# Optimization experiments

Measured on AMD Instinct MI355X. Metric: run time of the kernel, lower is better.

## Reference

```python
import jax, jax.numpy as jnp
import numpy as np

B, S, D, H = 4, 2048, 1024, 16
HD = D // H
EPS = 1e-7  # K.epsilon()


def setup_inputs() -> dict:
    key = jax.random.key(0)
    ks = jax.random.split(key, 5)
    scale = 1.0 / np.sqrt(D)  # keep projections numerically tame (glorot-ish)
    return {
        "x": jax.random.normal(ks[0], (B, S, D), dtype=jnp.float32),
        "Wq": jax.random.normal(ks[1], (D, D), dtype=jnp.float32) * scale,
        "bq": jnp.zeros((D,), dtype=jnp.float32),
        "Wk": jax.random.normal(ks[2], (D, D), dtype=jnp.float32) * scale,
        "bk": jnp.zeros((D,), dtype=jnp.float32),
        "Wv": jax.random.normal(ks[3], (D, D), dtype=jnp.float32) * scale,
        "bv": jnp.zeros((D,), dtype=jnp.float32),
        "Wo": jax.random.normal(ks[4], (D, D), dtype=jnp.float32) * scale,
        "bo": jnp.zeros((D,), dtype=jnp.float32),
    }


def _split_heads(t):
    # [B,S,D] -> [B,H,S,HD]
    return t.reshape(B, S, H, HD).transpose(0, 2, 1, 3)


def reference(x, Wq, bq, Wk, bk, Wv, bv, Wo, bo):
    relu = jax.nn.relu
    # projections with post-activation (keras layer applies activation to each mapping)
    q = _split_heads(relu(x @ Wq + bq))
    k = _split_heads(relu(x @ Wk + bk))
    v = _split_heads(relu(x @ Wv + bv))
    # scaled dot-product scores, scale = sqrt(head_dim)
    e = jnp.einsum("bhqd,bhkd->bhqk", q, k) / jnp.sqrt(jnp.asarray(HD, x.dtype))
    # exp with row max over ALL keys (before masking), as in the source
    e = jnp.exp(e - jnp.max(e, axis=-1, keepdims=True))
    # history_only: multiplicative causal mask applied AFTER exp
    causal = (jnp.arange(S)[None, :] <= jnp.arange(S)[:, None]).astype(x.dtype)
    e = e * causal  # broadcasts over [B,H,S,S]
    a = e / (jnp.sum(e, axis=-1, keepdims=True) + EPS)
    ctx = jnp.einsum("bhqk,bhkd->bhqd", a, v)
    y = ctx.transpose(0, 2, 1, 3).reshape(B, S, D)  # merge heads
    return relu(y @ Wo + bo)
```

## Files before the change

kernel.cpp:

```cpp
#include <hip/hip_runtime.h>
#include <hip/hip_bf16.h>
#include <cstdint>
#include <cstddef>

#define B_  4
#define S_  2048
#define D_  1024
#define H_  16
#define HD_ 64

typedef _Float16 half8  __attribute__((ext_vector_type(8)));
typedef _Float16 half4v __attribute__((ext_vector_type(4)));
typedef _Float16 half2v __attribute__((ext_vector_type(2)));
typedef float    f32x4  __attribute__((ext_vector_type(4)));
typedef unsigned int uint2v __attribute__((ext_vector_type(2)));
typedef unsigned int uint4v __attribute__((ext_vector_type(4)));

__device__ __forceinline__ void async_copy16(const void* g, void* l) {
    __builtin_amdgcn_global_load_lds(
        (const __attribute__((address_space(1))) unsigned int*)g,
        (__attribute__((address_space(3))) unsigned int*)l,
        16, 0, 0);
}

__device__ __forceinline__ half8 hscale8(half8 v, _Float16 s) {
    #pragma unroll
    for (int i = 0; i < 8; ++i) v[i] *= s;
    return v;
}

__device__ __forceinline__ unsigned int pack2(float a, float b) {
    half2v h = { (_Float16)a, (_Float16)b };
    return __builtin_bit_cast(unsigned int, h);
}


__global__ void cast_x_kernel(const float4* __restrict__ in, half4v* __restrict__ out, int n4) {
    int i = blockIdx.x * 256 + threadIdx.x;
    if (i < n4) {
        float4 v = in[i];
        half4v h = { (_Float16)v.x, (_Float16)v.y, (_Float16)v.z, (_Float16)v.w };
        out[i] = h;
    }
}

__global__ void transpose_cast4_kernel(
    const float* __restrict__ W0, const float* __restrict__ W1,
    const float* __restrict__ W2, const float* __restrict__ W3,
    _Float16* __restrict__ T0, _Float16* __restrict__ T1,
    _Float16* __restrict__ T2, _Float16* __restrict__ T3)
{
    __shared__ float tile[32][33];
    const float* Wsel[4] = { W0, W1, W2, W3 };
    _Float16*    Tsel[4] = { T0, T1, T2, T3 };
    const float* W  = Wsel[blockIdx.z];
    _Float16*    Wt = Tsel[blockIdx.z];
    const int bn = blockIdx.x * 32, bk = blockIdx.y * 32;
    const int tx = threadIdx.x, ty = threadIdx.y;
    #pragma unroll
    for (int i = 0; i < 32; i += 8)
        tile[ty + i][tx] = W[(size_t)(bk + ty + i) * D_ + bn + tx];
    __syncthreads();
    #pragma unroll
    for (int i = 0; i < 32; i += 8)
        Wt[(size_t)(bn + ty + i) * D_ + bk + tx] = (_Float16)tile[tx][ty + i];
}

template<int OUT_MODE>
__global__ __launch_bounds__(256, 2) void gemm_bt_kernel(
    const _Float16* __restrict__ A, const _Float16* __restrict__ Bt,
    const float* __restrict__ b0, const float* __restrict__ b1,
    const float* __restrict__ b2,
    void* __restrict__ C0, void* __restrict__ C1, void* __restrict__ C2,
    int M, int N, int K)
{
    __shared__ _Float16 As[128 * 64];
    __shared__ _Float16 Bs[128 * 64];
    const int tid  = threadIdx.x;
    const int wid  = tid >> 6, lane = tid & 63;
    const int lr   = lane & 15, lq = lane >> 4;
    const int m0   = blockIdx.x * 128, n0 = blockIdx.y * 128;
    const int wm   = (wid >> 1) * 64, wn = (wid & 1) * 64;
    const int srow = tid >> 3;
    const int csw  = ((tid & 7) ^ (srow & 7)) * 8;

    f32x4 acc[4][4] = {};

    for (int k0 = 0; k0 < K; k0 += 64) {
        __syncthreads();
        #pragma unroll
        for (int i = 0; i < 4; ++i) {
            async_copy16(A  + (size_t)(m0 + i * 32 + srow) * K + k0 + csw,
                         (char*)As + (i * 256 + wid * 64) * 16);
            async_copy16(Bt + (size_t)(n0 + i * 32 + srow) * K + k0 + csw,
                         (char*)Bs + (i * 256 + wid * 64) * 16);
        }
        __syncthreads();
        #pragma unroll
        for (int ks = 0; ks < 2; ++ks) {
            half8 af[4], bf[4];
            #pragma unroll
            for (int t = 0; t < 4; ++t) {
                af[t] = *(const half8*)(As + (wm + t * 16 + lr) * 64 + (((ks * 4 + lq) ^ (lr & 7)) * 8));
                bf[t] = *(const half8*)(Bs + (wn + t * 16 + lr) * 64 + (((ks * 4 + lq) ^ (lr & 7)) * 8));
            }
            #pragma unroll
            for (int mt = 0; mt < 4; ++mt)
                #pragma unroll
                for (int nt = 0; nt < 4; ++nt)
                    acc[mt][nt] = __builtin_amdgcn_mfma_f32_16x16x32_f16(
                        af[mt], bf[nt], acc[mt][nt], 0, 0, 0);
        }
    }

    const int seg = (OUT_MODE == 3) ? (n0 >> 10) : 0;
    const float* bp = (OUT_MODE == 3) ? (seg == 0 ? b0 : (seg == 1 ? b1 : b2)) : b0;

    #pragma unroll
    for (int mt = 0; mt < 4; ++mt) {
        const int row = m0 + wm + mt * 16 + lq * 4;
        #pragma unroll
        for (int nt = 0; nt < 4; ++nt) {
            const int col = n0 + wn + nt * 16 + lr;
            const int cl  = (OUT_MODE == 3) ? (col & 1023) : col;
            const float bb = bp[cl];
            if (OUT_MODE == 3 && seg == 2) {
                const int b = row >> 11, sq = row & 2047;
                const int h = cl >> 6, hd = cl & 63;
                half4v o;
                #pragma unroll
                for (int r = 0; r < 4; ++r) {
                    float v = acc[mt][nt][r] + bb;
                    o[r] = (_Float16)(v > 0.0f ? v : 0.0f);
                }
                *(half4v*)((_Float16*)C2 +
                           ((size_t)(b * 16 + h) * 64 + hd) * S_ + sq) = o;
            } else if (OUT_MODE == 3) {
                _Float16* dst = (_Float16*)(seg ? C1 : C0);
                #pragma unroll
                for (int r = 0; r < 4; ++r) {
                    float v = acc[mt][nt][r] + bb;
                    dst[(size_t)(row + r) * 1024 + cl] = (_Float16)(v > 0.0f ? v : 0.0f);
                }
            } else {
                #pragma unroll
                for (int r = 0; r < 4; ++r) {
                    float v = acc[mt][nt][r] + bb;
                    ((float*)C0)[(size_t)(row + r) * N + col] = v > 0.0f ? v : 0.0f;
                }
            }
        }
    }
}

__global__ __launch_bounds__(256, 3) void attn_kernel(
    const _Float16* __restrict__ Qg, const _Float16* __restrict__ Kg,
    const _Float16* __restrict__ Vtg, _Float16* __restrict__ Y)
{
    __shared__ _Float16 Ks[2][64 * 64];
    __shared__ _Float16 Vt[2][64 * 64];

    const int i  = blockIdx.x;
    const int bh = ((i & 7) << 3) | (i >> 7);
    const int tp = (i >> 3) & 15;
    const int b  = bh >> 4, h = bh & 15;
    const int tid = threadIdx.x, wid = tid >> 6, lane = tid & 63;
    const int lr = lane & 15, lq = lane >> 4;

    const size_t base  = ((size_t)b * S_) * D_ + (size_t)h * HD_;
    const _Float16* Vh = Vtg + (size_t)bh * 64 * S_;

    const int srow = tid >> 3;
    const int csw  = ((tid & 7) ^ (srow & 7)) * 8;

    const int qb[2] = { 64 * tp + 16 * wid, 2048 - 64 * (tp + 1) + 16 * wid };
    const int dk[2] = { tp, 31 - tp };
    const int nIter = 32 - tp;

    half8 aq[2][2];
    #pragma unroll
    for (int f = 0; f < 2; ++f) {
        const _Float16* qp = Qg + base + (size_t)(qb[f] + lr) * D_;
        aq[f][0] = hscale8(*(const half8*)(qp + lq * 8),      (_Float16)0.18033688f);
        aq[f][1] = hscale8(*(const half8*)(qp + 32 + lq * 8), (_Float16)0.18033688f);
    }

    float lsum[2] = {};
    f32x4 O[2][4] = {};
    half8 apf[2][2];

    auto issue_tile = [&](int kb) {
        const int bufi = kb & 1;
        #pragma unroll
        for (int ii = 0; ii < 2; ++ii) {
            async_copy16(Kg + base + (size_t)(kb * 64 + ii * 32 + srow) * D_ + csw,
                         (char*)Ks[bufi] + (ii * 256 + wid * 64) * 16);
            async_copy16(Vh + (size_t)(ii * 32 + srow) * S_ + kb * 64 + csw,
                         (char*)Vt[bufi] + (ii * 256 + wid * 64) * 16);
        }
    };

    issue_tile(0);

    for (int kb = 0; kb < nIter; ++kb) {
        const int cur = kb & 1;
        __syncthreads();
        if (kb + 1 < nIter) issue_tile(kb + 1);

        const _Float16* Kc = Ks[cur];
        const _Float16* Vc = Vt[cur];

        half8 kf[2][4];
        #pragma unroll
        for (int ks = 0; ks < 2; ++ks)
            #pragma unroll
            for (int tt = 0; tt < 4; ++tt)
                kf[ks][tt] = *(const half8*)(Kc + (tt * 16 + lr) * 64 + (((ks * 4 + lq) ^ (lr & 7)) * 8));

        #pragma unroll
        for (int f = 0; f < 2; ++f) {
            if (kb > dk[f]) continue;

            f32x4 sc[4] = {};
            #pragma unroll
            for (int ks = 0; ks < 2; ++ks)
                #pragma unroll
                for (int tt = 0; tt < 4; ++tt)
                    sc[tt] = __builtin_amdgcn_mfma_f32_16x16x32_f16(kf[ks][tt], aq[f][ks], sc[tt], 0, 0, 0);

            const bool diag = (kb == dk[f]);
            const int qg = qb[f] + lr;
            const int kbase = kb * 64 + lq * 4;
            float sum = 0.0f;
            unsigned int pk[4][2];
            #pragma unroll
            for (int tt = 0; tt < 4; ++tt) {
                float ev[4];
                #pragma unroll
                for (int r = 0; r < 4; ++r) {
                    float e = __builtin_amdgcn_exp2f(fminf(sc[tt][r] - 5.770780f, 15.8696f));
                    if (diag)
                        e = (kbase + tt * 16 + r <= qg) ? e : 0.0f;
                    ev[r] = e;
                    sum += e;
                }
                pk[tt][0] = pack2(ev[0], ev[1]);
                pk[tt][1] = pack2(ev[2], ev[3]);
            }
            lsum[f] += sum;

            #pragma unroll
            for (int ks = 0; ks < 2; ++ks) {
                uint2v s1 = __builtin_amdgcn_permlane32_swap(pk[2 * ks][0], pk[2 * ks + 1][0], false, false);
                uint2v s2 = __builtin_amdgcn_permlane16_swap(s1[0], s1[1], false, false);
                uint2v u1 = __builtin_amdgcn_permlane32_swap(pk[2 * ks][1], pk[2 * ks + 1][1], false, false);
                uint2v u2 = __builtin_amdgcn_permlane16_swap(u1[0], u1[1], false, false);
                uint4v d = { s2[0], u2[0], s2[1], u2[1] };
                apf[f][ks] = __builtin_bit_cast(half8, d);
            }
        }

        half8 bv[2][4];
        #pragma unroll
        for (int ks = 0; ks < 2; ++ks)
            #pragma unroll
            for (int tt = 0; tt < 4; ++tt)
                bv[ks][tt] = *(const half8*)(Vc + (tt * 16 + lr) * 64 + (((ks * 4 + lq) ^ (lr & 7)) * 8));

        #pragma unroll
        for (int f = 0; f < 2; ++f) {
            if (kb > dk[f]) continue;
            #pragma unroll
            for (int ks = 0; ks < 2; ++ks)
                #pragma unroll
                for (int tt = 0; tt < 4; ++tt)
                    O[f][tt] = __builtin_amdgcn_mfma_f32_16x16x32_f16(apf[f][ks], bv[ks][tt], O[f][tt], 0, 0, 0);
        }
    }

    #pragma unroll
    for (int f = 0; f < 2; ++f) {
        float tot = lsum[f];
        tot += __shfl_xor(tot, 16);
        tot += __shfl_xor(tot, 32);
        const int q0 = qb[f] + lq * 4;
        #pragma unroll
        for (int r = 0; r < 4; ++r) {
            const float inv = 1.0f / (__shfl(tot, lq * 4 + r) + 1e-7f);
            #pragma unroll
            for (int nt = 0; nt < 4; ++nt)
                Y[base + (size_t)(q0 + r) * D_ + nt * 16 + lr] = (_Float16)(O[f][nt][r] * inv);
        }
    }
}


extern "C" void kernel_launch(void* const* d_in, const int* in_sizes, int n_in,
                              void* d_out, int out_size, void* d_ws, size_t ws_size,
                              hipStream_t stream) {
    const float* x  = (const float*)d_in[0];
    const float* Wq = (const float*)d_in[1];
    const float* bq = (const float*)d_in[2];
    const float* Wk = (const float*)d_in[3];
    const float* bk = (const float*)d_in[4];
    const float* Wv = (const float*)d_in[5];
    const float* bv = (const float*)d_in[6];
    const float* Wo = (const float*)d_in[7];
    const float* bo = (const float*)d_in[8];

    char* ws = (char*)d_ws;
    _Float16* xh  = (_Float16*)ws;
    _Float16* wtq = (_Float16*)(ws + (size_t)16777216);
    _Float16* wtk = wtq + 1048576;
    _Float16* wtv = wtk + 1048576;
    _Float16* wto = wtv + 1048576;
    _Float16* Qh  = (_Float16*)(ws + (size_t)16777216 + 4 * (size_t)2097152);
    _Float16* Kh  = Qh + 8388608;
    _Float16* Vth = Kh + 8388608;
    _Float16* Yh  = Vth + 8388608;
    float* out = (float*)d_out;

    cast_x_kernel<<<8192, 256, 0, stream>>>((const float4*)x, (half4v*)xh, 2097152);
    transpose_cast4_kernel<<<dim3(32, 32, 4), dim3(32, 8), 0, stream>>>(
        Wq, Wk, Wv, Wo, wtq, wtk, wtv, wto);

    gemm_bt_kernel<3><<<dim3(64, 24), 256, 0, stream>>>(
        xh, wtq, bq, bk, bv, Qh, Kh, Vth, 8192, 3072, 1024);

    attn_kernel<<<1024, 256, 0, stream>>>(Qh, Kh, Vth, Yh);

    gemm_bt_kernel<0><<<dim3(64, 8), 256, 0, stream>>>(
        Yh, wto, bo, bo, bo, out, out, out, 8192, 1024, 1024);
}
```

Baseline: 252.9 us.

## Process four query tiles per attention block to reuse K/V tiles

Each attention block now handles four 16-row query fragments per wave (two low and two high causal-paired tiles) instead of two, halving the grid to 512 blocks and sharing every loaded K/V LDS tile across twice the query work. The V fragment loads are hoisted alongside K, the PV MFMA is fused into the per-fragment loop, and s_setprio brackets the MFMA bursts. This cuts global/LDS traffic per unit of work but raises register pressure (launch bounds relaxed from 3 to 2 waves per SIMD) and gives fewer blocks for load balancing.

```diff
diff --git a/kernel.cpp b/kernel.cpp
--- a/kernel.cpp
+++ b/kernel.cpp
@@ -153,7 +153,7 @@
     }
 }
 
-__global__ __launch_bounds__(256, 3) void attn_kernel(
+__global__ __launch_bounds__(256, 2) void attn_kernel(
     const _Float16* __restrict__ Qg, const _Float16* __restrict__ Kg,
     const _Float16* __restrict__ Vtg, _Float16* __restrict__ Y)
 {
@@ -161,8 +161,8 @@
     __shared__ _Float16 Vt[2][64 * 64];
 
     const int i  = blockIdx.x;
-    const int bh = ((i & 7) << 3) | (i >> 7);
-    const int tp = (i >> 3) & 15;
+    const int bh = ((i & 7) << 3) | (i >> 6);
+    const int p  = (i >> 3) & 7;
     const int b  = bh >> 4, h = bh & 15;
     const int tid = threadIdx.x, wid = tid >> 6, lane = tid & 63;
     const int lr = lane & 15, lq = lane >> 4;
@@ -173,21 +173,22 @@
     const int srow = tid >> 3;
     const int csw  = ((tid & 7) ^ (srow & 7)) * 8;
 
-    const int qb[2] = { 64 * tp + 16 * wid, 2048 - 64 * (tp + 1) + 16 * wid };
-    const int dk[2] = { tp, 31 - tp };
-    const int nIter = 32 - tp;
-
-    half8 aq[2][2];
-    #pragma unroll
-    for (int f = 0; f < 2; ++f) {
+    const int L = 128 * p, Hh = 1920 - 128 * p;
+    const int qb[4] = { L + 16 * wid, L + 64 + 16 * wid,
+                        Hh + 16 * wid, Hh + 64 + 16 * wid };
+    const int dk[4] = { 2 * p, 2 * p + 1, 30 - 2 * p, 31 - 2 * p };
+    const int nIter = 32 - 2 * p;
+
+    half8 aq[4][2];
+    #pragma unroll
+    for (int f = 0; f < 4; ++f) {
         const _Float16* qp = Qg + base + (size_t)(qb[f] + lr) * D_;
         aq[f][0] = hscale8(*(const half8*)(qp + lq * 8),      (_Float16)0.18033688f);
         aq[f][1] = hscale8(*(const half8*)(qp + 32 + lq * 8), (_Float16)0.18033688f);
     }
 
-    float lsum[2] = {};
-    f32x4 O[2][4] = {};
-    half8 apf[2][2];
+    float lsum[4] = {};
+    f32x4 O[4][4] = {};
 
     auto issue_tile = [&](int kb) {
         const int bufi = kb & 1;
@@ -210,23 +211,27 @@
         const _Float16* Kc = Ks[cur];
         const _Float16* Vc = Vt[cur];
 
-        half8 kf[2][4];
+        half8 kf[2][4], bv[2][4];
         #pragma unroll
         for (int ks = 0; ks < 2; ++ks)
             #pragma unroll
-            for (int tt = 0; tt < 4; ++tt)
+            for (int tt = 0; tt < 4; ++tt) {
                 kf[ks][tt] = *(const half8*)(Kc + (tt * 16 + lr) * 64 + (((ks * 4 + lq) ^ (lr & 7)) * 8));
-
-        #pragma unroll
-        for (int f = 0; f < 2; ++f) {
+                bv[ks][tt] = *(const half8*)(Vc + (tt * 16 + lr) * 64 + (((ks * 4 + lq) ^ (lr & 7)) * 8));
+            }
+
+        #pragma unroll
+        for (int f = 0; f < 4; ++f) {
             if (kb > dk[f]) continue;
 
             f32x4 sc[4] = {};
+            __builtin_amdgcn_s_setprio(1);
             #pragma unroll
             for (int ks = 0; ks < 2; ++ks)
                 #pragma unroll
                 for (int tt = 0; tt < 4; ++tt)
                     sc[tt] = __builtin_amdgcn_mfma_f32_16x16x32_f16(kf[ks][tt], aq[f][ks], sc[tt], 0, 0, 0);
+            __builtin_amdgcn_s_setprio(0);
 
             const bool diag = (kb == dk[f]);
             const int qg = qb[f] + lr;
@@ -249,6 +254,7 @@
             }
             lsum[f] += sum;
 
+            half8 ap[2];
             #pragma unroll
             for (int ks = 0; ks < 2; ++ks) {
                 uint2v s1 = __builtin_amdgcn_permlane32_swap(pk[2 * ks][0], pk[2 * ks + 1][0], false, false);
@@ -256,30 +262,21 @@
                 uint2v u1 = __builtin_amdgcn_permlane32_swap(pk[2 * ks][1], pk[2 * ks + 1][1], false, false);
                 uint2v u2 = __builtin_amdgcn_permlane16_swap(u1[0], u1[1], false, false);
                 uint4v d = { s2[0], u2[0], s2[1], u2[1] };
-                apf[f][ks] = __builtin_bit_cast(half8, d);
-            }
-        }
-
-        half8 bv[2][4];
-        #pragma unroll
-        for (int ks = 0; ks < 2; ++ks)
-            #pragma unroll
-            for (int tt = 0; tt < 4; ++tt)
-                bv[ks][tt] = *(const half8*)(Vc + (tt * 16 + lr) * 64 + (((ks * 4 + lq) ^ (lr & 7)) * 8));
-
-        #pragma unroll
-        for (int f = 0; f < 2; ++f) {
-            if (kb > dk[f]) continue;
+                ap[ks] = __builtin_bit_cast(half8, d);
+            }
+
+            __builtin_amdgcn_s_setprio(1);
             #pragma unroll
             for (int ks = 0; ks < 2; ++ks)
                 #pragma unroll
                 for (int tt = 0; tt < 4; ++tt)
-                    O[f][tt] = __builtin_amdgcn_mfma_f32_16x16x32_f16(apf[f][ks], bv[ks][tt], O[f][tt], 0, 0, 0);
-        }
-    }
-
-    #pragma unroll
-    for (int f = 0; f < 2; ++f) {
+                    O[f][tt] = __builtin_amdgcn_mfma_f32_16x16x32_f16(ap[ks], bv[ks][tt], O[f][tt], 0, 0, 0);
+            __builtin_amdgcn_s_setprio(0);
+        }
+    }
+
+    #pragma unroll
+    for (int f = 0; f < 4; ++f) {
         float tot = lsum[f];
         tot += __shfl_xor(tot, 16);
         tot += __shfl_xor(tot, 32);
@@ -327,7 +324,7 @@
     gemm_bt_kernel<3><<<dim3(64, 24), 256, 0, stream>>>(
         xh, wtq, bq, bk, bv, Qh, Kh, Vth, 8192, 3072, 1024);
 
-    attn_kernel<<<1024, 256, 0, stream>>>(Qh, Kh, Vth, Yh);
+    attn_kernel<<<512, 256, 0, stream>>>(Qh, Kh, Vth, Yh);
 
     gemm_bt_kernel<0><<<dim3(64, 8), 256, 0, stream>>>(
         Yh, wto, bo, bo, bo, out, out, out, 8192, 1024, 1024);
```

Result: faster. 246.2 us (-2.6%).
